# Performance work log

Measured on AMD Instinct MI355X. Metric: run time of the kernel, lower is better.

Reference implementation:

```python
import jax, jax.numpy as jnp
import numpy as np

EMBED = 1024
ATTN = 1024

def setup_inputs() -> dict:
    key = jax.random.key(0)
    k1, k2, k3, k4 = jax.random.split(key, 4)
    x = jax.random.normal(k1, (32, 2048, EMBED), dtype=jnp.float32)
    W = jax.random.normal(k2, (EMBED, ATTN), dtype=jnp.float32) / np.sqrt(EMBED)
    b = jax.random.normal(k3, (ATTN,), dtype=jnp.float32) * 0.01
    ctx = jax.random.normal(k4, (ATTN,), dtype=jnp.float32)
    return {"x": x, "W": W, "b": b, "ctx": ctx}

def reference(x, W, b, ctx):
    # scores: [B, S] = tanh(x @ W + b) . ctx
    h = jnp.tanh(jnp.einsum('bse,ea->bsa', x, W) + b)
    scores = jnp.einsum('bsa,a->bs', h, ctx)
    weights = jax.nn.softmax(scores, axis=1)            # softmax over seq dim
    return jnp.einsum('bse,bs->be', x, weights)          # weighted sum pooling
```

## Files before the change

### kernel.cpp

```cpp
#include <hip/hip_runtime.h>
#include <hip/hip_bf16.h>

typedef _Float16 half8 __attribute__((ext_vector_type(8)));
typedef _Float16 half4 __attribute__((ext_vector_type(4)));
typedef float floatx4 __attribute__((ext_vector_type(4)));

#define EMBED 1024
#define SEQ   2048
#define BATCH 32
#define M_TOT (BATCH * SEQ)
#define KDIM  1024
#define NDIM  1024

#define GLOAD16(g, l) __builtin_amdgcn_global_load_lds(                      \
    (const __attribute__((address_space(1))) void*)(g),                      \
    (__attribute__((address_space(3))) void*)(l), 16, 0, 0)

__global__ void transpose_w_kernel(const float* __restrict__ W,
                                   _Float16* __restrict__ Wt) {
    __shared__ float t[32][33];
    const int kt = blockIdx.x * 32;
    const int nt = blockIdx.y * 32;
    #pragma unroll
    for (int i = 0; i < 4; ++i)
        t[threadIdx.y + 8 * i][threadIdx.x] =
            W[(size_t)(kt + threadIdx.y + 8 * i) * NDIM + nt + threadIdx.x];
    __syncthreads();
    #pragma unroll
    for (int i = 0; i < 4; ++i)
        Wt[(size_t)(nt + threadIdx.y + 8 * i) * KDIM + kt + threadIdx.x] =
            (_Float16)t[threadIdx.x][threadIdx.y + 8 * i];
}

__global__ __launch_bounds__(256) void pack_w_kernel(const float* __restrict__ W,
                                                     _Float16* __restrict__ Bp) {
    const int flat = blockIdx.x * 256 + threadIdx.x;
    int t = flat;
    const int lane = t & 63; t >>= 6;
    const int nf   = t & 3;  t >>= 2;
    const int wn   = t & 1;  t >>= 1;
    const int kt   = t & 31; t >>= 5;
    const int bn   = t;
    const int col = bn * 128 + wn * 64 + nf * 16 + (lane & 15);
    const int k0  = kt * 32 + (lane >> 4) * 8;
    half8 h;
    #pragma unroll
    for (int j = 0; j < 8; ++j)
        h[j] = (_Float16)W[(size_t)(k0 + j) * NDIM + col];
    *(half8*)(Bp + (size_t)flat * 8) = h;
}

__global__ void zero_kernel(float* __restrict__ scores, float* __restrict__ out) {
    const int i = blockIdx.x * 256 + threadIdx.x;
    if (i < M_TOT) scores[i] = 0.0f;
    if (i < BATCH * EMBED) out[i] = 0.0f;
}

__global__ __launch_bounds__(256) void cvt_x_kernel(const float* __restrict__ x,
                                                    _Float16* __restrict__ x16) {
    const size_t stride = (size_t)gridDim.x * 256 * 8;
    for (size_t i = ((size_t)blockIdx.x * 256 + threadIdx.x) * 8;
         i < (size_t)M_TOT * KDIM; i += stride) {
        const float4 a = *(const float4*)(x + i);
        const float4 b = *(const float4*)(x + i + 4);
        half8 h;
        h[0] = (_Float16)a.x; h[1] = (_Float16)a.y; h[2] = (_Float16)a.z; h[3] = (_Float16)a.w;
        h[4] = (_Float16)b.x; h[5] = (_Float16)b.y; h[6] = (_Float16)b.z; h[7] = (_Float16)b.w;
        *(half8*)(x16 + i) = h;
    }
}

__global__ __launch_bounds__(256, 4) void score_gemm9(
    const _Float16* __restrict__ x16, const _Float16* __restrict__ Bp,
    const float* __restrict__ bias, const float* __restrict__ ctx,
    float* __restrict__ scores) {
    __shared__ _Float16 As[2][128 * 32];

    const int nb = ((blockIdx.x & 7) << 9) | (blockIdx.x >> 3);
    const int bm = nb >> 3;
    const int bn = nb & 7;
    const int tid = threadIdx.x;
    const int lane = tid & 63;
    const int wid = tid >> 6;
    const int wm = wid >> 1;
    const int wn = wid & 1;

    const int jA0 = wid;
    const int lrow = lane >> 2;
    const int gslot = (lane & 3) ^ ((lane >> 3) & 3);
    const int gcol = gslot * 8;

    const _Float16* Ab = x16 + (size_t)(bm * 128) * KDIM;

    floatx4 acc[4][4] = {};

    const int frow = lane & 15;
    const int fslot = ((lane >> 4) ^ ((frow >> 1) & 3)) * 8;

    #define STAGE(buf, kt)                                                        \
        {                                                                         \
            const int kc = (kt) * 32 + gcol;                                      \
            _Pragma("unroll")                                                     \
            for (int i = 0; i < 2; ++i) {                                         \
                const int j = jA0 + i * 4;                                        \
                GLOAD16(Ab + (size_t)(j * 16 + lrow) * KDIM + kc, &As[buf][j * 512]); \
            }                                                                     \
        }

    const int4* Bp4 = (const int4*)Bp;
    #define BLOAD(dst, kt)                                                        \
        {                                                                         \
            const int4* p = Bp4 + ((((size_t)bn * 32 + (kt)) * 2 + wn) * 4) * 64 + lane; \
            dst[0] = p[0]; dst[1] = p[64]; dst[2] = p[128]; dst[3] = p[192];      \
        }

    int4 Bcur[4], Bnext[4];

    STAGE(0, 0);
    BLOAD(Bcur, 0);
    __syncthreads();

    for (int kt = 0; kt < KDIM / 32; ++kt) {
        const int cur = kt & 1;
        if (kt + 1 < KDIM / 32) {
            STAGE(cur ^ 1, kt + 1);
            BLOAD(Bnext, kt + 1);
        }

        half8 afr[4];
        #pragma unroll
        for (int m = 0; m < 4; ++m)
            afr[m] = *(const half8*)&As[cur][(wm * 64 + m * 16 + frow) * 32 + fslot];

        #pragma unroll
        for (int m = 0; m < 4; ++m)
            #pragma unroll
            for (int n = 0; n < 4; ++n)
                acc[m][n] = __builtin_amdgcn_mfma_f32_16x16x32_f16(
                    afr[m], *(const half8*)&Bcur[n], acc[m][n], 0, 0, 0);

        __syncthreads();
        #pragma unroll
        for (int n = 0; n < 4; ++n) Bcur[n] = Bnext[n];
    }
    #undef BLOAD
    #undef STAGE

    float bv[4], cv[4];
    #pragma unroll
    for (int n = 0; n < 4; ++n) {
        const int col = bn * 128 + wn * 64 + n * 16 + (lane & 15);
        bv[n] = bias[col];
        cv[n] = ctx[col];
    }
    #pragma unroll
    for (int m = 0; m < 4; ++m) {
        #pragma unroll
        for (int j = 0; j < 4; ++j) {
            float partial = 0.0f;
            #pragma unroll
            for (int n = 0; n < 4; ++n) {
                const float v = acc[m][n][j] + bv[n];
                const float e = __expf(2.0f * v);
                const float t = 1.0f - 2.0f * __builtin_amdgcn_rcpf(e + 1.0f);
                partial += t * cv[n];
            }
            #pragma unroll
            for (int off = 1; off < 16; off <<= 1)
                partial += __shfl_xor(partial, off, 64);
            if ((lane & 15) == 0) {
                const int rowg = bm * 128 + wm * 64 + m * 16 + (lane >> 4) * 4 + j;
                atomicAdd(&scores[rowg], partial);
            }
        }
    }
}

__global__ __launch_bounds__(256) void score_gemm_f32(
    const float* __restrict__ A32p, const _Float16* __restrict__ Wt,
    const float* __restrict__ bias, const float* __restrict__ ctx,
    float* __restrict__ scores) {
    __shared__ _Float16 As[128 * 64];
    __shared__ _Float16 Bs[128 * 64];

    const int bid = blockIdx.x;
    const int bm = bid >> 3;
    const int bn = bid & 7;
    const int tid = threadIdx.x;
    const int lane = tid & 63;
    const int wid = tid >> 6;
    const int wm = wid >> 1;
    const int wn = wid & 1;

    const int c = tid & 7;
    const int r0 = tid >> 3;
    const int swz = (r0 & 7) << 3;
    const int wcol = (c * 8) ^ swz;

    float4 aF[4][2];
    int4   bR[4];

    #pragma unroll
    for (int i = 0; i < 4; ++i) {
        const int row = r0 + 32 * i;
        const float* p = A32p + (size_t)(bm * 128 + row) * KDIM + c * 8;
        aF[i][0] = *(const float4*)p;
        aF[i][1] = *(const float4*)(p + 4);
        bR[i] = *(const int4*)(Wt + (size_t)(bn * 128 + row) * KDIM + c * 8);
    }

    floatx4 acc[4][4] = {};

    for (int kt = 0; kt < KDIM / 64; ++kt) {
        __syncthreads();
        #pragma unroll
        for (int i = 0; i < 4; ++i) {
            const int row = r0 + 32 * i;
            half8 h;
            h[0] = (_Float16)aF[i][0].x; h[1] = (_Float16)aF[i][0].y;
            h[2] = (_Float16)aF[i][0].z; h[3] = (_Float16)aF[i][0].w;
            h[4] = (_Float16)aF[i][1].x; h[5] = (_Float16)aF[i][1].y;
            h[6] = (_Float16)aF[i][1].z; h[7] = (_Float16)aF[i][1].w;
            *(half8*)&As[row * 64 + wcol] = h;
            *(int4*)&Bs[row * 64 + wcol] = bR[i];
        }
        __syncthreads();

        if (kt + 1 < KDIM / 64) {
            #pragma unroll
            for (int i = 0; i < 4; ++i) {
                const int row = r0 + 32 * i;
                const float* p = A32p + (size_t)(bm * 128 + row) * KDIM + (kt + 1) * 64 + c * 8;
                aF[i][0] = *(const float4*)p;
                aF[i][1] = *(const float4*)(p + 4);
                bR[i] = *(const int4*)(Wt + (size_t)(bn * 128 + row) * KDIM + (kt + 1) * 64 + c * 8);
            }
        }

        #pragma unroll
        for (int s = 0; s < 2; ++s) {
            half8 afr[4], bfr[4];
            const int colr = s * 32 + (lane >> 4) * 8;
            #pragma unroll
            for (int m = 0; m < 4; ++m) {
                const int row = wm * 64 + m * 16 + (lane & 15);
                afr[m] = *(const half8*)&As[row * 64 + (colr ^ ((row & 7) << 3))];
            }
            #pragma unroll
            for (int n = 0; n < 4; ++n) {
                const int row = wn * 64 + n * 16 + (lane & 15);
                bfr[n] = *(const half8*)&Bs[row * 64 + (colr ^ ((row & 7) << 3))];
            }
            #pragma unroll
            for (int m = 0; m < 4; ++m)
                #pragma unroll
                for (int n = 0; n < 4; ++n)
                    acc[m][n] = __builtin_amdgcn_mfma_f32_16x16x32_f16(
                        afr[m], bfr[n], acc[m][n], 0, 0, 0);
        }
    }

    float bv[4], cv[4];
    #pragma unroll
    for (int n = 0; n < 4; ++n) {
        const int col = bn * 128 + wn * 64 + n * 16 + (lane & 15);
        bv[n] = bias[col];
        cv[n] = ctx[col];
    }
    #pragma unroll
    for (int m = 0; m < 4; ++m) {
        #pragma unroll
        for (int j = 0; j < 4; ++j) {
            float partial = 0.0f;
            #pragma unroll
            for (int n = 0; n < 4; ++n) {
                const float v = acc[m][n][j] + bv[n];
                const float e = __expf(2.0f * v);
                const float t = 1.0f - 2.0f * __builtin_amdgcn_rcpf(e + 1.0f);
                partial += t * cv[n];
            }
            #pragma unroll
            for (int off = 1; off < 16; off <<= 1)
                partial += __shfl_xor(partial, off, 64);
            if ((lane & 15) == 0) {
                const int rowg = bm * 128 + wm * 64 + m * 16 + (lane >> 4) * 4 + j;
                atomicAdd(&scores[rowg], partial);
            }
        }
    }
}

__global__ void softmax_kernel(const float* __restrict__ scores,
                               float* __restrict__ weights) {
    const int bb = blockIdx.x;
    const int tid = threadIdx.x;
    const float* s = scores + (size_t)bb * SEQ;
    float* w = weights + (size_t)bb * SEQ;

    __shared__ float red[8];

    float v[8];
    float mx = -1e30f;
    #pragma unroll
    for (int i = 0; i < 8; ++i) {
        v[i] = s[tid + i * 256];
        mx = fmaxf(mx, v[i]);
    }
    #pragma unroll
    for (int off = 1; off < 64; off <<= 1)
        mx = fmaxf(mx, __shfl_xor(mx, off, 64));
    const int wv = tid >> 6;
    if ((tid & 63) == 0) red[wv] = mx;
    __syncthreads();
    mx = fmaxf(fmaxf(red[0], red[1]), fmaxf(red[2], red[3]));

    float sum = 0.0f;
    #pragma unroll
    for (int i = 0; i < 8; ++i) {
        v[i] = __expf(v[i] - mx);
        sum += v[i];
    }
    #pragma unroll
    for (int off = 1; off < 64; off <<= 1)
        sum += __shfl_xor(sum, off, 64);
    if ((tid & 63) == 0) red[4 + wv] = sum;
    __syncthreads();
    sum = red[4] + red[5] + red[6] + red[7];
    const float inv = 1.0f / sum;
    #pragma unroll
    for (int i = 0; i < 8; ++i)
        w[tid + i * 256] = v[i] * inv;
}

__global__ __launch_bounds__(256) void pool_kernel(const float* __restrict__ x,
                                                   const float* __restrict__ weights,
                                                   float* __restrict__ out) {
    const int bb = blockIdx.x >> 4;
    const int sc = blockIdx.x & 15;
    const int tid = threadIdx.x;

    const float4* xb = (const float4*)(x + (size_t)bb * SEQ * EMBED) +
                       (size_t)(sc * 128) * (EMBED / 4) + tid;
    const float* wb = weights + (size_t)bb * SEQ + sc * 128;

    float ax = 0.f, ay = 0.f, az = 0.f, aw = 0.f;
    #pragma unroll 4
    for (int s = 0; s < 128; ++s) {
        const float wgt = wb[s];
        const float4 xv = xb[(size_t)s * (EMBED / 4)];
        ax += wgt * xv.x; ay += wgt * xv.y; az += wgt * xv.z; aw += wgt * xv.w;
    }
    float* o = out + (size_t)bb * EMBED + tid * 4;
    atomicAdd(o + 0, ax);
    atomicAdd(o + 1, ay);
    atomicAdd(o + 2, az);
    atomicAdd(o + 3, aw);
}

__global__ __launch_bounds__(256) void pool16_kernel(const _Float16* __restrict__ x16,
                                                     const float* __restrict__ weights,
                                                     float* __restrict__ out) {
    const int bb = blockIdx.x >> 4;
    const int sc = blockIdx.x & 15;
    const int tid = threadIdx.x;

    const _Float16* xb = x16 + (size_t)bb * SEQ * EMBED +
                         (size_t)(sc * 128) * EMBED + tid * 4;
    const float* wb = weights + (size_t)bb * SEQ + sc * 128;

    float ax = 0.f, ay = 0.f, az = 0.f, aw = 0.f;
    #pragma unroll 4
    for (int s = 0; s < 128; ++s) {
        const float wgt = wb[s];
        const half4 h = *(const half4*)(xb + (size_t)s * EMBED);
        ax += wgt * (float)h[0]; ay += wgt * (float)h[1];
        az += wgt * (float)h[2]; aw += wgt * (float)h[3];
    }
    float* o = out + (size_t)bb * EMBED + tid * 4;
    atomicAdd(o + 0, ax);
    atomicAdd(o + 1, ay);
    atomicAdd(o + 2, az);
    atomicAdd(o + 3, aw);
}

extern "C" void kernel_launch(void* const* d_in, const int* in_sizes, int n_in,
                              void* d_out, int out_size, void* d_ws, size_t ws_size,
                              hipStream_t stream) {
    const float* x   = (const float*)d_in[0];
    const float* W   = (const float*)d_in[1];
    const float* b   = (const float*)d_in[2];
    const float* ctx = (const float*)d_in[3];
    float* out = (float*)d_out;

    char* ws = (char*)d_ws;
    _Float16* Bp      = (_Float16*)ws;
    _Float16* Wt      = (_Float16*)ws;
    float*    scores  = (float*)(ws + (2u << 20));
    float*    weights = (float*)(ws + (2u << 20) + (256u << 10));
    _Float16* x16     = (_Float16*)(ws + (4u << 20));

    const size_t need = (4ull << 20) + ((size_t)M_TOT * KDIM * 2);
    const bool fast = ws_size >= need;

    hipLaunchKernelGGL(zero_kernel, dim3(M_TOT / 256), dim3(256), 0, stream, scores, out);

    if (fast) {
        hipLaunchKernelGGL(pack_w_kernel, dim3(512), dim3(256), 0, stream, W, Bp);
        hipLaunchKernelGGL(cvt_x_kernel, dim3(4096), dim3(256), 0, stream, x, x16);
        hipLaunchKernelGGL(score_gemm9, dim3(4096), dim3(256), 0, stream,
                           x16, Bp, b, ctx, scores);
    } else {
        hipLaunchKernelGGL(transpose_w_kernel, dim3(32, 32), dim3(32, 8), 0, stream, W, Wt);
        hipLaunchKernelGGL(score_gemm_f32, dim3(4096), dim3(256), 0, stream,
                           x, Wt, b, ctx, scores);
    }

    hipLaunchKernelGGL(softmax_kernel, dim3(BATCH), dim3(256), 0, stream, scores, weights);

    if (fast) {
        hipLaunchKernelGGL(pool16_kernel, dim3(BATCH * 16), dim3(256), 0, stream,
                           x16, weights, out);
    } else {
        hipLaunchKernelGGL(pool_kernel, dim3(BATCH * 16), dim3(256), 0, stream,
                           x, weights, out);
    }
}
```

Baseline: 287.4 us.

## Load GEMM A fragments directly from global into registers, dropping LDS staging

```diff
diff --git a/kernel.cpp b/kernel.cpp
--- a/kernel.cpp
+++ b/kernel.cpp
@@ -11,10 +11,6 @@
 #define M_TOT (BATCH * SEQ)
 #define KDIM  1024
 #define NDIM  1024
-
-#define GLOAD16(g, l) __builtin_amdgcn_global_load_lds(                      \
-    (const __attribute__((address_space(1))) void*)(g),                      \
-    (__attribute__((address_space(3))) void*)(l), 16, 0, 0)
 
 __global__ void transpose_w_kernel(const float* __restrict__ W,
                                    _Float16* __restrict__ Wt) {
@@ -70,12 +66,10 @@
     }
 }
 
-__global__ __launch_bounds__(256, 4) void score_gemm9(
+__global__ __launch_bounds__(256, 3) void score_gemm10(
     const _Float16* __restrict__ x16, const _Float16* __restrict__ Bp,
     const float* __restrict__ bias, const float* __restrict__ ctx,
     float* __restrict__ scores) {
-    __shared__ _Float16 As[2][128 * 32];
-
     const int nb = ((blockIdx.x & 7) << 9) | (blockIdx.x >> 3);
     const int bm = nb >> 3;
     const int bn = nb & 7;
@@ -85,66 +79,39 @@
     const int wm = wid >> 1;
     const int wn = wid & 1;
 
-    const int jA0 = wid;
-    const int lrow = lane >> 2;
-    const int gslot = (lane & 3) ^ ((lane >> 3) & 3);
-    const int gcol = gslot * 8;
-
-    const _Float16* Ab = x16 + (size_t)(bm * 128) * KDIM;
+    const _Float16* Abase = x16 +
+        (size_t)(bm * 128 + wm * 64 + (lane & 15)) * KDIM + (lane >> 4) * 8;
+    const int4* Bbase = (const int4*)Bp + ((size_t)(bn * 64 + wn) * 4) * 64 + lane;
 
     floatx4 acc[4][4] = {};
-
-    const int frow = lane & 15;
-    const int fslot = ((lane >> 4) ^ ((frow >> 1) & 3)) * 8;
-
-    #define STAGE(buf, kt)                                                        \
-        {                                                                         \
-            const int kc = (kt) * 32 + gcol;                                      \
-            _Pragma("unroll")                                                     \
-            for (int i = 0; i < 2; ++i) {                                         \
-                const int j = jA0 + i * 4;                                        \
-                GLOAD16(Ab + (size_t)(j * 16 + lrow) * KDIM + kc, &As[buf][j * 512]); \
-            }                                                                     \
-        }
-
-    const int4* Bp4 = (const int4*)Bp;
-    #define BLOAD(dst, kt)                                                        \
-        {                                                                         \
-            const int4* p = Bp4 + ((((size_t)bn * 32 + (kt)) * 2 + wn) * 4) * 64 + lane; \
-            dst[0] = p[0]; dst[1] = p[64]; dst[2] = p[128]; dst[3] = p[192];      \
-        }
-
-    int4 Bcur[4], Bnext[4];
-
-    STAGE(0, 0);
-    BLOAD(Bcur, 0);
-    __syncthreads();
-
-    for (int kt = 0; kt < KDIM / 32; ++kt) {
-        const int cur = kt & 1;
-        if (kt + 1 < KDIM / 32) {
-            STAGE(cur ^ 1, kt + 1);
-            BLOAD(Bnext, kt + 1);
-        }
-
-        half8 afr[4];
-        #pragma unroll
-        for (int m = 0; m < 4; ++m)
-            afr[m] = *(const half8*)&As[cur][(wm * 64 + m * 16 + frow) * 32 + fslot];
-
-        #pragma unroll
-        for (int m = 0; m < 4; ++m)
-            #pragma unroll
-            for (int n = 0; n < 4; ++n)
-                acc[m][n] = __builtin_amdgcn_mfma_f32_16x16x32_f16(
-                    afr[m], *(const half8*)&Bcur[n], acc[m][n], 0, 0, 0);
-
-        __syncthreads();
-        #pragma unroll
-        for (int n = 0; n < 4; ++n) Bcur[n] = Bnext[n];
-    }
-    #undef BLOAD
-    #undef STAGE
+    int4 A0[4], A1[4], B0[4], B1[4];
+
+    #define LDA(dst, kt)                                                         \
+        { _Pragma("unroll")                                                      \
+          for (int m = 0; m < 4; ++m)                                            \
+              dst[m] = *(const int4*)(Abase + (size_t)(kt) * 32 + m * 16 * KDIM); }
+    #define LDB(dst, kt)                                                         \
+        { const int4* p = Bbase + (size_t)(kt) * 512;                            \
+          _Pragma("unroll")                                                      \
+          for (int n = 0; n < 4; ++n) dst[n] = p[n * 64]; }
+    #define COMP(A, B)                                                           \
+        { _Pragma("unroll")                                                      \
+          for (int m = 0; m < 4; ++m)                                            \
+              _Pragma("unroll")                                                  \
+              for (int n = 0; n < 4; ++n)                                        \
+                  acc[m][n] = __builtin_amdgcn_mfma_f32_16x16x32_f16(            \
+                      *(const half8*)&A[m], *(const half8*)&B[n], acc[m][n], 0, 0, 0); }
+
+    LDA(A0, 0); LDB(B0, 0);
+    for (int kt = 0; kt < KDIM / 32; kt += 2) {
+        LDA(A1, kt + 1); LDB(B1, kt + 1);
+        COMP(A0, B0);
+        if (kt + 2 < KDIM / 32) { LDA(A0, kt + 2); LDB(B0, kt + 2); }
+        COMP(A1, B1);
+    }
+    #undef COMP
+    #undef LDB
+    #undef LDA
 
     float bv[4], cv[4];
     #pragma unroll
@@ -407,7 +374,7 @@
     if (fast) {
         hipLaunchKernelGGL(pack_w_kernel, dim3(512), dim3(256), 0, stream, W, Bp);
         hipLaunchKernelGGL(cvt_x_kernel, dim3(4096), dim3(256), 0, stream, x, x16);
-        hipLaunchKernelGGL(score_gemm9, dim3(4096), dim3(256), 0, stream,
+        hipLaunchKernelGGL(score_gemm10, dim3(4096), dim3(256), 0, stream,
                            x16, Bp, b, ctx, scores);
     } else {
         hipLaunchKernelGGL(transpose_w_kernel, dim3(32, 32), dim3(32, 8), 0, stream, W, Wt);
```

After: 427.0 us. 48.6% more time.

## Fuse fp32-to-fp16 conversion of x into score GEMM and drop x16 buffer

Applied to the files above, without the earlier changes.

```diff
diff --git a/kernel.cpp b/kernel.cpp
--- a/kernel.cpp
+++ b/kernel.cpp
@@ -56,25 +56,11 @@
     if (i < BATCH * EMBED) out[i] = 0.0f;
 }
 
-__global__ __launch_bounds__(256) void cvt_x_kernel(const float* __restrict__ x,
-                                                    _Float16* __restrict__ x16) {
-    const size_t stride = (size_t)gridDim.x * 256 * 8;
-    for (size_t i = ((size_t)blockIdx.x * 256 + threadIdx.x) * 8;
-         i < (size_t)M_TOT * KDIM; i += stride) {
-        const float4 a = *(const float4*)(x + i);
-        const float4 b = *(const float4*)(x + i + 4);
-        half8 h;
-        h[0] = (_Float16)a.x; h[1] = (_Float16)a.y; h[2] = (_Float16)a.z; h[3] = (_Float16)a.w;
-        h[4] = (_Float16)b.x; h[5] = (_Float16)b.y; h[6] = (_Float16)b.z; h[7] = (_Float16)b.w;
-        *(half8*)(x16 + i) = h;
-    }
-}
-
-__global__ __launch_bounds__(256, 4) void score_gemm9(
-    const _Float16* __restrict__ x16, const _Float16* __restrict__ Bp,
+__global__ __launch_bounds__(256, 4) void score_gemm11(
+    const float* __restrict__ x, const _Float16* __restrict__ Bp,
     const float* __restrict__ bias, const float* __restrict__ ctx,
     float* __restrict__ scores) {
-    __shared__ _Float16 As[2][128 * 32];
+    __shared__ float Asf[2][128 * 32];
 
     const int nb = ((blockIdx.x & 7) << 9) | (blockIdx.x >> 3);
     const int bm = nb >> 3;
@@ -85,64 +71,80 @@
     const int wm = wid >> 1;
     const int wn = wid & 1;
 
-    const int jA0 = wid;
-    const int lrow = lane >> 2;
-    const int gslot = (lane & 3) ^ ((lane >> 3) & 3);
-    const int gcol = gslot * 8;
-
-    const _Float16* Ab = x16 + (size_t)(bm * 128) * KDIM;
+    const int srow = lane >> 3;
+    const int gslA = (lane & 7) ^ srow;
+    const float* Ab = x + (size_t)(bm * 128) * KDIM;
 
     floatx4 acc[4][4] = {};
 
     const int frow = lane & 15;
-    const int fslot = ((lane >> 4) ^ ((frow >> 1) & 3)) * 8;
+    const int fhi  = lane >> 4;
+    const int fx   = frow & 7;
 
     #define STAGE(buf, kt)                                                        \
         {                                                                         \
-            const int kc = (kt) * 32 + gcol;                                      \
             _Pragma("unroll")                                                     \
-            for (int i = 0; i < 2; ++i) {                                         \
-                const int j = jA0 + i * 4;                                        \
-                GLOAD16(Ab + (size_t)(j * 16 + lrow) * KDIM + kc, &As[buf][j * 512]); \
+            for (int i = 0; i < 4; ++i) {                                         \
+                const int j = wid + i * 4;                                        \
+                GLOAD16(Ab + (size_t)(j * 8 + srow) * KDIM + (kt) * 32 + gslA * 4,\
+                        &Asf[buf][(j * 8) * 32]);                                 \
             }                                                                     \
         }
 
-    const int4* Bp4 = (const int4*)Bp;
+    const int4* Bp4 = (const int4*)Bp + ((size_t)(bn * 64 + wn) * 4) * 64 + lane;
     #define BLOAD(dst, kt)                                                        \
         {                                                                         \
-            const int4* p = Bp4 + ((((size_t)bn * 32 + (kt)) * 2 + wn) * 4) * 64 + lane; \
+            const int4* p = Bp4 + (size_t)(kt) * 512;                             \
             dst[0] = p[0]; dst[1] = p[64]; dst[2] = p[128]; dst[3] = p[192];      \
         }
 
-    int4 Bcur[4], Bnext[4];
+    #define COMPUTE(buf, B)                                                       \
+        {                                                                         \
+            half8 afr[4];                                                         \
+            _Pragma("unroll")                                                     \
+            for (int m = 0; m < 4; ++m) {                                         \
+                const int r = wm * 64 + m * 16 + frow;                            \
+                const floatx4 f0 = *(const floatx4*)&Asf[buf][r * 32 +            \
+                                        (((2 * fhi) ^ fx) * 4)];                  \
+                const floatx4 f1 = *(const floatx4*)&Asf[buf][r * 32 +            \
+                                        (((2 * fhi + 1) ^ fx) * 4)];              \
+                half8 a;                                                          \
+                a[0] = (_Float16)f0[0]; a[1] = (_Float16)f0[1];                   \
+                a[2] = (_Float16)f0[2]; a[3] = (_Float16)f0[3];                   \
+                a[4] = (_Float16)f1[0]; a[5] = (_Float16)f1[1];                   \
+                a[6] = (_Float16)f1[2]; a[7] = (_Float16)f1[3];                   \
+                afr[m] = a;                                                       \
+            }                                                                     \
+            __builtin_amdgcn_s_setprio(1);                                        \
+            _Pragma("unroll")                                                     \
+            for (int m = 0; m < 4; ++m)                                           \
+                _Pragma("unroll")                                                 \
+                for (int n = 0; n < 4; ++n)                                       \
+                    acc[m][n] = __builtin_amdgcn_mfma_f32_16x16x32_f16(           \
+                        afr[m], *(const half8*)&B[n], acc[m][n], 0, 0, 0);        \
+            __builtin_amdgcn_s_setprio(0);                                        \
+        }
+
+    int4 B0[4], B1[4];
 
     STAGE(0, 0);
-    BLOAD(Bcur, 0);
+    BLOAD(B0, 0);
     __syncthreads();
 
-    for (int kt = 0; kt < KDIM / 32; ++kt) {
-        const int cur = kt & 1;
-        if (kt + 1 < KDIM / 32) {
-            STAGE(cur ^ 1, kt + 1);
-            BLOAD(Bnext, kt + 1);
-        }
-
-        half8 afr[4];
-        #pragma unroll
-        for (int m = 0; m < 4; ++m)
-            afr[m] = *(const half8*)&As[cur][(wm * 64 + m * 16 + frow) * 32 + fslot];
-
-        #pragma unroll
-        for (int m = 0; m < 4; ++m)
-            #pragma unroll
-            for (int n = 0; n < 4; ++n)
-                acc[m][n] = __builtin_amdgcn_mfma_f32_16x16x32_f16(
-                    afr[m], *(const half8*)&Bcur[n], acc[m][n], 0, 0, 0);
-
+    for (int kt2 = 0; kt2 < 16; ++kt2) {
+        const int kte = kt2 * 2;
+        STAGE(1, kte + 1);
+        BLOAD(B1, kte + 1);
+        COMPUTE(0, B0);
         __syncthreads();
-        #pragma unroll
-        for (int n = 0; n < 4; ++n) Bcur[n] = Bnext[n];
-    }
+        if (kte + 2 < 32) {
+            STAGE(0, kte + 2);
+            BLOAD(B0, kte + 2);
+        }
+        COMPUTE(1, B1);
+        __syncthreads();
+    }
+    #undef COMPUTE
     #undef BLOAD
     #undef STAGE
 
@@ -357,32 +359,6 @@
     atomicAdd(o + 3, aw);
 }
 
-__global__ __launch_bounds__(256) void pool16_kernel(const _Float16* __restrict__ x16,
-                                                     const float* __restrict__ weights,
-                                                     float* __restrict__ out) {
-    const int bb = blockIdx.x >> 4;
-    const int sc = blockIdx.x & 15;
-    const int tid = threadIdx.x;
-
-    const _Float16* xb = x16 + (size_t)bb * SEQ * EMBED +
-                         (size_t)(sc * 128) * EMBED + tid * 4;
-    const float* wb = weights + (size_t)bb * SEQ + sc * 128;
-
-    float ax = 0.f, ay = 0.f, az = 0.f, aw = 0.f;
-    #pragma unroll 4
-    for (int s = 0; s < 128; ++s) {
-        const float wgt = wb[s];
-        const half4 h = *(const half4*)(xb + (size_t)s * EMBED);
-        ax += wgt * (float)h[0]; ay += wgt * (float)h[1];
-        az += wgt * (float)h[2]; aw += wgt * (float)h[3];
-    }
-    float* o = out + (size_t)bb * EMBED + tid * 4;
-    atomicAdd(o + 0, ax);
-    atomicAdd(o + 1, ay);
-    atomicAdd(o + 2, az);
-    atomicAdd(o + 3, aw);
-}
-
 extern "C" void kernel_launch(void* const* d_in, const int* in_sizes, int n_in,
                               void* d_out, int out_size, void* d_ws, size_t ws_size,
                               hipStream_t stream) {
@@ -397,18 +373,16 @@
     _Float16* Wt      = (_Float16*)ws;
     float*    scores  = (float*)(ws + (2u << 20));
     float*    weights = (float*)(ws + (2u << 20) + (256u << 10));
-    _Float16* x16     = (_Float16*)(ws + (4u << 20));
-
-    const size_t need = (4ull << 20) + ((size_t)M_TOT * KDIM * 2);
+
+    const size_t need = (4ull << 20);
     const bool fast = ws_size >= need;
 
     hipLaunchKernelGGL(zero_kernel, dim3(M_TOT / 256), dim3(256), 0, stream, scores, out);
 
     if (fast) {
         hipLaunchKernelGGL(pack_w_kernel, dim3(512), dim3(256), 0, stream, W, Bp);
-        hipLaunchKernelGGL(cvt_x_kernel, dim3(4096), dim3(256), 0, stream, x, x16);
-        hipLaunchKernelGGL(score_gemm9, dim3(4096), dim3(256), 0, stream,
-                           x16, Bp, b, ctx, scores);
+        hipLaunchKernelGGL(score_gemm11, dim3(4096), dim3(256), 0, stream,
+                           x, Bp, b, ctx, scores);
     } else {
         hipLaunchKernelGGL(transpose_w_kernel, dim3(32, 32), dim3(32, 8), 0, stream, W, Wt);
         hipLaunchKernelGGL(score_gemm_f32, dim3(4096), dim3(256), 0, stream,
@@ -416,12 +390,6 @@
     }
 
     hipLaunchKernelGGL(softmax_kernel, dim3(BATCH), dim3(256), 0, stream, scores, weights);
-
-    if (fast) {
-        hipLaunchKernelGGL(pool16_kernel, dim3(BATCH * 16), dim3(256), 0, stream,
-                           x16, weights, out);
-    } else {
-        hipLaunchKernelGGL(pool_kernel, dim3(BATCH * 16), dim3(256), 0, stream,
-                           x, weights, out);
-    }
-}
+    hipLaunchKernelGGL(pool_kernel, dim3(BATCH * 16), dim3(256), 0, stream,
+                       x, weights, out);
+}
```

Measured after the change: 527.5 us. +83.5%, slower.
